# Performance work log

Hardware: AMD Instinct MI355X
Metric: run time of the kernel (lower is better)

## Reference

```python
import jax, jax.numpy as jnp
import numpy as np

B, T, D, H = 4, 1024, 1024, 16
DK = D // H
SCALE = float(np.sqrt(DK))


def setup_inputs() -> dict:
    key = jax.random.key(0)
    ks = jax.random.split(key, 12)
    std = 1.0 / np.sqrt(D)
    inp = {
        "x": jax.random.normal(ks[0], (B, T, D), dtype=jnp.float32),
        "s2_distances": jax.random.uniform(ks[1], (B, T, T), dtype=jnp.float32),
        # causal mask: 1 where attention allowed (j <= i)
        "mask": jnp.broadcast_to(jnp.tril(jnp.ones((T, T), dtype=jnp.int32)), (B, T, T)),
        "Wq": jax.random.uniform(ks[2], (D, D), jnp.float32, -std, std),
        "bq": jax.random.uniform(ks[3], (D,), jnp.float32, -std, std),
        "Wk": jax.random.uniform(ks[4], (D, D), jnp.float32, -std, std),
        "bk": jax.random.uniform(ks[5], (D,), jnp.float32, -std, std),
        "Wv": jax.random.uniform(ks[6], (D, D), jnp.float32, -std, std),
        "bv": jax.random.uniform(ks[7], (D,), jnp.float32, -std, std),
        "Wo": jax.random.uniform(ks[8], (D, D), jnp.float32, -std, std),
        "bo": jax.random.uniform(ks[9], (D,), jnp.float32, -std, std),
        "spatial_weight": jnp.float32(0.5),
    }
    return inp


def reference(x, s2_distances, mask, Wq, bq, Wk, bk, Wv, bv, Wo, bo, spatial_weight):
    b, t, _ = x.shape
    # projections: torch nn.Linear is x @ W.T + b
    def proj(W, bias):
        y = jnp.einsum("btd,ed->bte", x, W) + bias
        return y.reshape(b, t, H, DK).transpose(0, 2, 1, 3)  # [B,H,T,dk]

    Q, K, V = proj(Wq, bq), proj(Wk, bk), proj(Wv, bv)
    # scores: QK^T/sqrt(dk) - |alpha| * dist  (dist broadcast over heads)
    scores = jnp.einsum("bhqd,bhkd->bhqk", Q, K) / SCALE
    scores = scores - jnp.abs(spatial_weight) * s2_distances[:, None, :, :]
    scores = jnp.where(mask[:, None, :, :] == 0, -jnp.inf, scores)
    probs = jax.nn.softmax(scores, axis=-1)
    out = jnp.einsum("bhqk,bhkd->bhqd", probs, V)
    out = out.transpose(0, 2, 1, 3).reshape(b, t, D)
    return jnp.einsum("btd,ed->bte", out, Wo) + bo
```

## Files before the change

kernel.cpp:

```cpp
#include <hip/hip_runtime.h>
#include <stdint.h>

#define Tt 1024
#define Dd 1024
#define Hh 16
#define NT 32

typedef unsigned short u16;
typedef __attribute__((ext_vector_type(8))) short short8;
typedef __attribute__((ext_vector_type(4))) float f32x4;
typedef __attribute__((ext_vector_type(4))) unsigned short u16x4;

typedef const __attribute__((address_space(1))) uint32_t* gptr_t;
typedef __attribute__((address_space(3))) uint32_t* lptr_t;

#define QSCALE 0.18033688011112042f
#define LOG2E 1.4426950408889634f

static __device__ __forceinline__ u16 f2bf(float f) {
  union { float f; unsigned u; } x;
  x.f = f;
  unsigned u = x.u;
  return (u16)((u + 0x7fffu + ((u >> 16) & 1u)) >> 16);
}

static __device__ __forceinline__ u16 f2bf_fast(float f) {
  union { float f; unsigned u; } x;
  x.f = f;
  return (u16)((x.u + 0x8000u) >> 16);
}

static __device__ __forceinline__ float bf2f(u16 u) {
  union { unsigned u; float f; } x;
  x.u = ((unsigned)u) << 16;
  return x.f;
}

static __device__ __forceinline__ float fexp2(float x) {
#if __has_builtin(__builtin_amdgcn_exp2f)
  return __builtin_amdgcn_exp2f(x);
#else
  return exp2f(x);
#endif
}

__global__ __launch_bounds__(256) void cvt_kernel(
    const float* __restrict__ x, const float* __restrict__ wq,
    const float* __restrict__ wk, const float* __restrict__ wv,
    const float* __restrict__ wo, u16* __restrict__ xb, u16* __restrict__ wb) {
  size_t i = ((size_t)blockIdx.x * 256 + threadIdx.x) * 4;
  const size_t XN = (size_t)4 * 1024 * 1024;
  const float* src;
  u16* dst;
  size_t off;
  if (i < XN) {
    src = x; dst = xb; off = i;
  } else {
    size_t j = i - XN;
    int wi = (int)(j >> 20);
    src = (wi == 0) ? wq : (wi == 1) ? wk : (wi == 2) ? wv : wo;
    dst = wb + ((size_t)wi << 20);
    off = j & ((1u << 20) - 1);
  }
  float4 v = *(const float4*)(src + off);
  u16x4 o;
  o.x = f2bf(v.x); o.y = f2bf(v.y); o.z = f2bf(v.z); o.w = f2bf(v.w);
  *(u16x4*)(dst + off) = o;
}

__global__ __launch_bounds__(512, 2) void qkv_fused_kernel(
    const u16* __restrict__ xb, const u16* __restrict__ wb,
    const float* __restrict__ bq, const float* __restrict__ bk,
    const float* __restrict__ bv, u16* __restrict__ Q, u16* __restrict__ Kk,
    u16* __restrict__ Vt, const float* __restrict__ dist,
    const float* __restrict__ alphap, u16* __restrict__ biasb) {
  __shared__ u16 lds[65536];
  const int bid = blockIdx.x;
  const int xcd = bid & 7, cslot = bid >> 3;
  if (cslot >= 24) {
    const int cid = xcd * 8 + (cslot - 24);
    const float scl = -fabsf(alphap[0]) * LOG2E;
    const size_t idx = (size_t)cid * 512 + threadIdx.x;
#pragma unroll 4
    for (int i = 0; i < 32; i++) {
      const size_t off = idx * 4 + (size_t)i * 131072;
      float4 v = *(const float4*)(dist + off);
      u16x4 o;
      o.x = f2bf(v.x * scl); o.y = f2bf(v.y * scl);
      o.z = f2bf(v.z * scl); o.w = f2bf(v.w * scl);
      *(u16x4*)(biasb + off) = o;
    }
    return;
  }
  const int gid = xcd * 24 + cslot;
  const int mt = gid / 12, ny = gid - mt * 12;
  const int z = ny >> 2;
  const int m0 = mt * 256, nc = (ny & 3) * 256;
  const u16* W = wb + ((size_t)z << 20);

  const int t = threadIdx.x, w = t >> 6, l = t & 63;
  const int quad = l >> 4, l15 = l & 15;
  const int wr = w >> 2, wn = w & 3;
  char* ldc = (char*)lds;

  const int srow = t >> 2;
  const int scw = ((t & 3) ^ ((srow >> 1) & 3)) * 8;
  const u16* gA = xb + (size_t)(m0 + srow) * Dd + scw;
  const u16* gB = W + (size_t)(nc + srow) * Dd + scw;
  const int lb = w * 1024;

  auto stageA = [&](int kt, int u) {
    __builtin_amdgcn_global_load_lds(
        (gptr_t)(gA + (size_t)u * 128 * Dd + kt * 32),
        (lptr_t)(ldc + (kt & 3) * 32768 + u * 8192 + lb), 16, 0, 0);
  };
  auto stageB = [&](int kt, int u) {
    __builtin_amdgcn_global_load_lds(
        (gptr_t)(gB + (size_t)u * 128 * Dd + kt * 32),
        (lptr_t)(ldc + (kt & 3) * 32768 + 16384 + u * 8192 + lb), 16, 0, 0);
  };

  f32x4 acc[8][4];
#pragma unroll
  for (int i = 0; i < 8; i++)
#pragma unroll
    for (int j = 0; j < 4; j++) acc[i][j] = (f32x4){0.f, 0.f, 0.f, 0.f};

#pragma unroll
  for (int p = 0; p < 3; p++) {
    stageA(p, 0); stageA(p, 1); stageB(p, 0); stageB(p, 1);
  }
  asm volatile("s_waitcnt vmcnt(8)" ::: "memory");
  __builtin_amdgcn_s_barrier();

  const int rsw = (quad ^ ((l15 >> 1) & 3)) * 16;
  const int aoff = wr * 8192 + l15 * 64 + rsw;
  const int boff = 16384 + wn * 4096 + l15 * 64 + rsw;

#pragma unroll 1
  for (int kt = 0; kt < NT; kt++) {
    const char* sl = ldc + (kt & 3) * 32768;
    short8 af[4], bfv[4];
#pragma unroll
    for (int i = 0; i < 4; i++) af[i] = *(const short8*)(sl + aoff + i * 1024);
#pragma unroll
    for (int i = 0; i < 4; i++) bfv[i] = *(const short8*)(sl + boff + i * 1024);
    if (kt + 3 < NT) { stageA(kt + 3, 0); stageA(kt + 3, 1); }
    __builtin_amdgcn_s_barrier();
    asm volatile("s_waitcnt lgkmcnt(0)" ::: "memory");
    __builtin_amdgcn_sched_barrier(0);
    __builtin_amdgcn_s_setprio(1);
#pragma unroll
    for (int mi = 0; mi < 4; mi++)
#pragma unroll
      for (int ni = 0; ni < 4; ni++)
        acc[mi][ni] = __builtin_amdgcn_mfma_f32_16x16x32_bf16(
            af[mi], bfv[ni], acc[mi][ni], 0, 0, 0);
    __builtin_amdgcn_s_setprio(0);
    __builtin_amdgcn_s_barrier();
#pragma unroll
    for (int i = 0; i < 4; i++)
      af[i] = *(const short8*)(sl + aoff + 4096 + i * 1024);
    if (kt + 3 < NT) { stageB(kt + 3, 0); stageB(kt + 3, 1); }
    if (kt < NT - 3) {
      asm volatile("s_waitcnt vmcnt(8)" ::: "memory");
    } else if (kt == NT - 3) {
      asm volatile("s_waitcnt vmcnt(4)" ::: "memory");
    } else if (kt == NT - 2) {
      asm volatile("s_waitcnt vmcnt(0)" ::: "memory");
    }
    __builtin_amdgcn_s_barrier();
    asm volatile("s_waitcnt lgkmcnt(0)" ::: "memory");
    __builtin_amdgcn_sched_barrier(0);
    __builtin_amdgcn_s_setprio(1);
#pragma unroll
    for (int mi = 0; mi < 4; mi++)
#pragma unroll
      for (int ni = 0; ni < 4; ni++)
        acc[mi + 4][ni] = __builtin_amdgcn_mfma_f32_16x16x32_bf16(
            af[mi], bfv[ni], acc[mi + 4][ni], 0, 0, 0);
    __builtin_amdgcn_s_setprio(0);
    __builtin_amdgcn_s_barrier();
  }

  const float* bias = (z == 0) ? bq : (z == 1) ? bk : bv;
  const float scl = (z == 0) ? QSCALE : 1.0f;
  if (z < 2) {
#pragma unroll
    for (int mi = 0; mi < 8; mi++)
#pragma unroll
      for (int ni = 0; ni < 4; ni++) {
        const int n = wn * 64 + ni * 16 + l15;
        const float bn = bias[nc + n];
#pragma unroll
        for (int r = 0; r < 4; r++) {
          const int m = wr * 128 + mi * 16 + quad * 4 + r;
          lds[m * 256 + n] = f2bf((acc[mi][ni][r] + bn) * scl);
        }
      }
  } else {
#pragma unroll
    for (int mi = 0; mi < 8; mi++)
#pragma unroll
      for (int ni = 0; ni < 4; ni++) {
        const int n = wn * 64 + ni * 16 + l15;
        const float bn = bias[nc + n];
        u16x4 o;
        o.x = f2bf(acc[mi][ni][0] + bn);
        o.y = f2bf(acc[mi][ni][1] + bn);
        o.z = f2bf(acc[mi][ni][2] + bn);
        o.w = f2bf(acc[mi][ni][3] + bn);
        *(u16x4*)&lds[n * 256 + wr * 128 + mi * 16 + quad * 4] = o;
      }
  }
  __syncthreads();
  const int row = t >> 5;
  const int chunk = (t & 31) * 8;
  if (z < 2) {
    u16* out = (z == 0) ? Q : Kk;
#pragma unroll
    for (int it = 0; it < 16; it++) {
      const int rr = it * 16 + row;
      *(short8*)(out + (size_t)(m0 + rr) * Dd + nc + chunk) =
          *(const short8*)&lds[rr * 256 + chunk];
    }
  } else {
    const int b2 = m0 >> 10, t0 = m0 & (Tt - 1);
#pragma unroll
    for (int it = 0; it < 16; it++) {
      const int rr = it * 16 + row;
      *(short8*)(Vt + ((size_t)b2 * Dd + nc + rr) * Tt + t0 + chunk) =
          *(const short8*)&lds[rr * 256 + chunk];
    }
  }
}

__global__ __launch_bounds__(512) void gemm_out_kernel(
    const u16* __restrict__ Ao, const u16* __restrict__ Wo,
    const float* __restrict__ bo, float* __restrict__ out) {
  __shared__ u16 lds[2 * 12288];
  const int m0 = blockIdx.x * 128, n0 = blockIdx.y * 64;
  const int t = threadIdx.x, w = t >> 6, l = t & 63, quad = l >> 4, l15 = l & 15;
  const int srow = t >> 3;
  const int scol = ((l & 7) ^ ((l >> 3) & 7)) * 8;
  const u16* ga = Ao + (size_t)(m0 + srow) * Dd + scol;
  const u16* gb = Wo + (size_t)(n0 + srow) * Dd + scol;
  char* ldc = (char*)lds;
  const int xr = l15 & 7;
  f32x4 acc[4];
#pragma unroll
  for (int j = 0; j < 4; j++) acc[j] = (f32x4){0.f, 0.f, 0.f, 0.f};

  auto stage = [&](int k0, int buf) {
    char* base = ldc + buf * 24576 + w * 1024;
#pragma unroll
    for (int i = 0; i < 2; i++)
      __builtin_amdgcn_global_load_lds((gptr_t)(ga + k0 + (size_t)i * 64 * Dd),
                                       (lptr_t)(base + i * 8192), 16, 0, 0);
    __builtin_amdgcn_global_load_lds((gptr_t)(gb + k0),
                                     (lptr_t)(base + 16384), 16, 0, 0);
  };

  stage(0, 0);
#pragma unroll 1
  for (int it = 0; it < Dd / 64; it++) {
    const int buf = it & 1;
    __builtin_amdgcn_s_waitcnt(0);
    __syncthreads();
    if (it + 1 < Dd / 64) stage((it + 1) * 64, buf ^ 1);
    const u16* lA = lds + buf * 12288;
    const u16* lB = lA + 8192;
#pragma unroll
    for (int kk = 0; kk < 2; kk++) {
      const int cs = ((kk * 4 + quad) ^ xr) * 8;
      const short8 af = *(const short8*)(lA + (w * 16 + l15) * 64 + cs);
#pragma unroll
      for (int ni = 0; ni < 4; ni++) {
        const short8 bfr = *(const short8*)(lB + (ni * 16 + l15) * 64 + cs);
        acc[ni] = __builtin_amdgcn_mfma_f32_16x16x32_bf16(af, bfr, acc[ni], 0, 0, 0);
      }
    }
  }
#pragma unroll
  for (int ni = 0; ni < 4; ni++) {
    const int n = n0 + ni * 16 + l15;
    const float bn = bo[n];
#pragma unroll
    for (int r = 0; r < 4; r++) {
      const int m = m0 + w * 16 + quad * 4 + r;
      out[(size_t)m * Dd + n] = acc[ni][r] + bn;
    }
  }
}

__global__ __launch_bounds__(256) void attn_kernel(
    const u16* __restrict__ Q, const u16* __restrict__ Kk,
    const u16* __restrict__ Vt, const u16* __restrict__ biasb,
    u16* __restrict__ Oo) {
  __shared__ u16 lK[2][64 * 64];
  __shared__ u16 lV[2][64 * 64];
  __shared__ u16 lPp[4][16 * 64];
  const int t = threadIdx.x, w = t >> 6, l = t & 63, quad = l >> 4, l15 = l & 15;
  const int g = blockIdx.x >> 8;
  const int j = (blockIdx.x >> 6) & 3;
  const int bh = blockIdx.x & 63;
  const int qb = (g == 0) ? 15 - j : (g == 1) ? 8 + j : (g == 2) ? 7 - j : j;
  const int h = bh & (Hh - 1), b = bh >> 4;
  const int q0 = qb * 64;

  const int srow = w * 8 + (l >> 3);
  const int schunk = ((l & 7) ^ ((l >> 3) & 7)) * 8;
  const u16* gK = Kk + ((size_t)b * Tt + srow) * Dd + h * 64 + schunk;
  const u16* gV = Vt + ((size_t)b * Dd + h * 64 + srow) * Tt + schunk;
  char* lKc0 = (char*)&lK[0][0];
  char* lVc0 = (char*)&lV[0][0];
  const int wbase = w * 1024;

  auto stage = [&](int k0, int buf) {
#pragma unroll
    for (int i = 0; i < 2; i++) {
      __builtin_amdgcn_global_load_lds(
          (gptr_t)(gK + (size_t)(k0 + i * 32) * Dd),
          (lptr_t)(lKc0 + buf * 8192 + wbase + i * 4096), 16, 0, 0);
      __builtin_amdgcn_global_load_lds(
          (gptr_t)(gV + (size_t)(i * 32) * Tt + k0),
          (lptr_t)(lVc0 + buf * 8192 + wbase + i * 4096), 16, 0, 0);
    }
  };

  const int qrow = q0 + w * 16 + l15;
  const u16* Qp = Q + ((size_t)b * Tt + qrow) * Dd + h * 64 + quad * 8;
  const short8 qf0 = *(const short8*)Qp;
  const short8 qf1 = *(const short8*)(Qp + 32);
  const u16* bp = biasb + ((size_t)b * Tt + qrow) * Tt + quad * 4;

  const int xr = l15 & 7;
  u16* lpr = &lPp[w][l15 * 64];
  const int niter = qb + 1;

  f32x4 oacc[4];
#pragma unroll
  for (int dt = 0; dt < 4; dt++) oacc[dt] = (f32x4){0.f, 0.f, 0.f, 0.f};
  f32x4 lsum4 = (f32x4){0.f, 0.f, 0.f, 0.f};
  u16x4 bbA[4], bbB[4];

  stage(0, 0);
#pragma unroll
  for (int nt = 0; nt < 4; nt++) bbA[nt] = *(const u16x4*)(bp + nt * 16);

#pragma unroll 1
  for (int kt = 0; kt < niter; kt++) {
    const int buf = kt & 1;
    __builtin_amdgcn_s_waitcnt(0);
    __syncthreads();
    if (kt + 1 < niter) {
      stage((kt + 1) * 64, buf ^ 1);
#pragma unroll
      for (int nt = 0; nt < 4; nt++)
        bbB[nt] = *(const u16x4*)(bp + (kt + 1) * 64 + nt * 16);
    }
    f32x4 sacc[4];
#pragma unroll
    for (int nt = 0; nt < 4; nt++) {
#pragma unroll
      for (int r = 0; r < 4; r++) sacc[nt][r] = bf2f(bbA[nt][r]);
    }
#pragma unroll
    for (int ks = 0; ks < 2; ks++) {
      const short8 qf = ks ? qf1 : qf0;
      const int cs = ((ks * 4 + quad) ^ xr) * 8;
#pragma unroll
      for (int nt = 0; nt < 4; nt++) {
        const short8 kf = *(const short8*)&lK[buf][(nt * 16 + l15) * 64 + cs];
        sacc[nt] = __builtin_amdgcn_mfma_f32_16x16x32_bf16(kf, qf, sacc[nt], 0, 0, 0);
      }
    }
    if (kt == qb) {
      const int kbase = kt * 64 + quad * 4;
#pragma unroll
      for (int nt = 0; nt < 4; nt++) {
        u16x4 pk;
#pragma unroll
        for (int r = 0; r < 4; r++) {
          const float p = (kbase + nt * 16 + r <= qrow) ? fexp2(sacc[nt][r]) : 0.f;
          lsum4[nt] += p;
          pk[r] = f2bf_fast(p);
        }
        *(u16x4*)&lpr[((nt * 4 + quad) ^ (xr << 1)) * 4] = pk;
      }
    } else {
#pragma unroll
      for (int nt = 0; nt < 4; nt++) {
        u16x4 pk;
#pragma unroll
        for (int r = 0; r < 4; r++) {
          const float p = fexp2(sacc[nt][r]);
          lsum4[nt] += p;
          pk[r] = f2bf_fast(p);
        }
        *(u16x4*)&lpr[((nt * 4 + quad) ^ (xr << 1)) * 4] = pk;
      }
    }
#pragma unroll
    for (int ks = 0; ks < 2; ks++) {
      const int cs = ((ks * 4 + quad) ^ xr) * 8;
      const short8 pa = *(const short8*)&lpr[cs];
#pragma unroll
      for (int dt = 0; dt < 4; dt++) {
        const short8 vf = *(const short8*)&lV[buf][(dt * 16 + l15) * 64 + cs];
        oacc[dt] = __builtin_amdgcn_mfma_f32_16x16x32_bf16(pa, vf, oacc[dt], 0, 0, 0);
      }
    }
#pragma unroll
    for (int nt = 0; nt < 4; nt++) bbA[nt] = bbB[nt];
  }

  float lsum = (lsum4[0] + lsum4[1]) + (lsum4[2] + lsum4[3]);
  lsum += __shfl_xor(lsum, 16);
  lsum += __shfl_xor(lsum, 32);
  const float inv = 1.0f / lsum;
  float invq[4];
#pragma unroll
  for (int r = 0; r < 4; r++) invq[r] = __shfl(inv, quad * 4 + r);
#pragma unroll
  for (int dt = 0; dt < 4; dt++) {
#pragma unroll
    for (int r = 0; r < 4; r++) {
      Oo[((size_t)b * Tt + q0 + w * 16 + quad * 4 + r) * Dd + h * 64 + dt * 16 + l15] =
          f2bf(oacc[dt][r] * invq[r]);
    }
  }
}

extern "C" void kernel_launch(void* const* d_in, const int* in_sizes, int n_in,
                              void* d_out, int out_size, void* d_ws, size_t ws_size,
                              hipStream_t stream) {
  const float* x = (const float*)d_in[0];
  const float* dist = (const float*)d_in[1];
  const float* Wq = (const float*)d_in[3];
  const float* bq = (const float*)d_in[4];
  const float* Wk = (const float*)d_in[5];
  const float* bk = (const float*)d_in[6];
  const float* Wv = (const float*)d_in[7];
  const float* bv = (const float*)d_in[8];
  const float* Wo = (const float*)d_in[9];
  const float* bo = (const float*)d_in[10];
  const float* alphap = (const float*)d_in[11];

  char* ws = (char*)d_ws;
  u16* xb = (u16*)(ws);
  u16* wb = (u16*)(ws + ((size_t)8 << 20));
  u16* Qb = (u16*)(ws + ((size_t)16 << 20));
  u16* Kb = (u16*)(ws + ((size_t)24 << 20));
  u16* Vtb = (u16*)(ws + ((size_t)32 << 20));
  u16* biasb = (u16*)(ws + ((size_t)40 << 20));
  u16* Ob = xb;
  float* outp = (float*)d_out;

  cvt_kernel<<<8192, 256, 0, stream>>>(x, Wq, Wk, Wv, Wo, xb, wb);
  qkv_fused_kernel<<<256, 512, 0, stream>>>(xb, wb, bq, bk, bv, Qb, Kb, Vtb,
                                            dist, alphap, biasb);
  attn_kernel<<<1024, 256, 0, stream>>>(Qb, Kb, Vtb, biasb, Ob);
  dim3 g2(32, 16);
  gemm_out_kernel<<<g2, 512, 0, stream>>>(Ob, wb + ((size_t)3 << 20), bo, outp);
}
```

Measured before the change: 194.9 us.

## Move distance-bias conversion into cvt kernel and restructure QKV GEMM pipeline

The fp32-to-bf16 conversion of the scaled distance bias moves out of the QKV GEMM kernel's extra blocks and into the elementwise cvt kernel, which gets a larger grid. The QKV GEMM switches from a 4-stage K=32 ring with split A/B staging to a double-buffered K=64 tile with an XOR-swizzled 128-byte row layout. Its LDS epilogue stores are also swizzled to reduce bank conflicts. The prefetch depth drops from three tiles to one, so global latency may be less well hidden, while barrier overhead per K step is lower.

```diff
diff --git a/kernel.cpp b/kernel.cpp
--- a/kernel.cpp
+++ b/kernel.cpp
@@ -4,7 +4,6 @@
 #define Tt 1024
 #define Dd 1024
 #define Hh 16
-#define NT 32
 
 typedef unsigned short u16;
 typedef __attribute__((ext_vector_type(8))) short short8;
@@ -47,24 +46,32 @@
 __global__ __launch_bounds__(256) void cvt_kernel(
     const float* __restrict__ x, const float* __restrict__ wq,
     const float* __restrict__ wk, const float* __restrict__ wv,
-    const float* __restrict__ wo, u16* __restrict__ xb, u16* __restrict__ wb) {
+    const float* __restrict__ wo, const float* __restrict__ dist,
+    const float* __restrict__ alphap, u16* __restrict__ xb,
+    u16* __restrict__ wb, u16* __restrict__ biasb) {
   size_t i = ((size_t)blockIdx.x * 256 + threadIdx.x) * 4;
   const size_t XN = (size_t)4 * 1024 * 1024;
+  const size_t WN = (size_t)8 * 1024 * 1024;
+  float mul = 1.0f;
   const float* src;
   u16* dst;
   size_t off;
   if (i < XN) {
     src = x; dst = xb; off = i;
-  } else {
+  } else if (i < WN) {
     size_t j = i - XN;
     int wi = (int)(j >> 20);
     src = (wi == 0) ? wq : (wi == 1) ? wk : (wi == 2) ? wv : wo;
     dst = wb + ((size_t)wi << 20);
     off = j & ((1u << 20) - 1);
+  } else {
+    src = dist; dst = biasb; off = i - WN;
+    mul = -fabsf(alphap[0]) * LOG2E;
   }
   float4 v = *(const float4*)(src + off);
   u16x4 o;
-  o.x = f2bf(v.x); o.y = f2bf(v.y); o.z = f2bf(v.z); o.w = f2bf(v.w);
+  o.x = f2bf(v.x * mul); o.y = f2bf(v.y * mul);
+  o.z = f2bf(v.z * mul); o.w = f2bf(v.w * mul);
   *(u16x4*)(dst + off) = o;
 }
 
@@ -72,28 +79,10 @@
     const u16* __restrict__ xb, const u16* __restrict__ wb,
     const float* __restrict__ bq, const float* __restrict__ bk,
     const float* __restrict__ bv, u16* __restrict__ Q, u16* __restrict__ Kk,
-    u16* __restrict__ Vt, const float* __restrict__ dist,
-    const float* __restrict__ alphap, u16* __restrict__ biasb) {
+    u16* __restrict__ Vt) {
   __shared__ u16 lds[65536];
   const int bid = blockIdx.x;
-  const int xcd = bid & 7, cslot = bid >> 3;
-  if (cslot >= 24) {
-    const int cid = xcd * 8 + (cslot - 24);
-    const float scl = -fabsf(alphap[0]) * LOG2E;
-    const size_t idx = (size_t)cid * 512 + threadIdx.x;
-#pragma unroll 4
-    for (int i = 0; i < 32; i++) {
-      const size_t off = idx * 4 + (size_t)i * 131072;
-      float4 v = *(const float4*)(dist + off);
-      u16x4 o;
-      o.x = f2bf(v.x * scl); o.y = f2bf(v.y * scl);
-      o.z = f2bf(v.z * scl); o.w = f2bf(v.w * scl);
-      *(u16x4*)(biasb + off) = o;
-    }
-    return;
-  }
-  const int gid = xcd * 24 + cslot;
-  const int mt = gid / 12, ny = gid - mt * 12;
+  const int mt = bid & 15, ny = bid >> 4;
   const int z = ny >> 2;
   const int m0 = mt * 256, nc = (ny & 3) * 256;
   const u16* W = wb + ((size_t)z << 20);
@@ -103,22 +92,23 @@
   const int wr = w >> 2, wn = w & 3;
   char* ldc = (char*)lds;
 
-  const int srow = t >> 2;
-  const int scw = ((t & 3) ^ ((srow >> 1) & 3)) * 8;
-  const u16* gA = xb + (size_t)(m0 + srow) * Dd + scw;
-  const u16* gB = W + (size_t)(nc + srow) * Dd + scw;
+  const int srow = t >> 3;
+  const int schunk = ((t & 7) ^ (srow & 7)) * 8;
+  const u16* gA = xb + (size_t)(m0 + srow) * Dd + schunk;
+  const u16* gB = W + (size_t)(nc + srow) * Dd + schunk;
   const int lb = w * 1024;
 
-  auto stageA = [&](int kt, int u) {
-    __builtin_amdgcn_global_load_lds(
-        (gptr_t)(gA + (size_t)u * 128 * Dd + kt * 32),
-        (lptr_t)(ldc + (kt & 3) * 32768 + u * 8192 + lb), 16, 0, 0);
+  auto stage = [&](int kt, int buf) {
+#pragma unroll
+    for (int u = 0; u < 4; u++) {
+      __builtin_amdgcn_global_load_lds(
+          (gptr_t)(gA + (size_t)u * 64 * Dd + kt * 64),
+          (lptr_t)(ldc + buf * 65536 + u * 8192 + lb), 16, 0, 0);
+      __builtin_amdgcn_global_load_lds(
+          (gptr_t)(gB + (size_t)u * 64 * Dd + kt * 64),
+          (lptr_t)(ldc + buf * 65536 + 32768 + u * 8192 + lb), 16, 0, 0);
+    }
   };
-  auto stageB = [&](int kt, int u) {
-    __builtin_amdgcn_global_load_lds(
-        (gptr_t)(gB + (size_t)u * 128 * Dd + kt * 32),
-        (lptr_t)(ldc + (kt & 3) * 32768 + 16384 + u * 8192 + lb), 16, 0, 0);
-  };
 
   f32x4 acc[8][4];
 #pragma unroll
@@ -126,61 +116,41 @@
 #pragma unroll
     for (int j = 0; j < 4; j++) acc[i][j] = (f32x4){0.f, 0.f, 0.f, 0.f};
 
-#pragma unroll
-  for (int p = 0; p < 3; p++) {
-    stageA(p, 0); stageA(p, 1); stageB(p, 0); stageB(p, 1);
-  }
-  asm volatile("s_waitcnt vmcnt(8)" ::: "memory");
+  stage(0, 0);
+  asm volatile("s_waitcnt vmcnt(0)" ::: "memory");
   __builtin_amdgcn_s_barrier();
 
-  const int rsw = (quad ^ ((l15 >> 1) & 3)) * 16;
-  const int aoff = wr * 8192 + l15 * 64 + rsw;
-  const int boff = 16384 + wn * 4096 + l15 * 64 + rsw;
+  const int xr = l15 & 7;
 
 #pragma unroll 1
-  for (int kt = 0; kt < NT; kt++) {
-    const char* sl = ldc + (kt & 3) * 32768;
-    short8 af[4], bfv[4];
-#pragma unroll
-    for (int i = 0; i < 4; i++) af[i] = *(const short8*)(sl + aoff + i * 1024);
-#pragma unroll
-    for (int i = 0; i < 4; i++) bfv[i] = *(const short8*)(sl + boff + i * 1024);
-    if (kt + 3 < NT) { stageA(kt + 3, 0); stageA(kt + 3, 1); }
-    __builtin_amdgcn_s_barrier();
-    asm volatile("s_waitcnt lgkmcnt(0)" ::: "memory");
-    __builtin_amdgcn_sched_barrier(0);
-    __builtin_amdgcn_s_setprio(1);
-#pragma unroll
-    for (int mi = 0; mi < 4; mi++)
+  for (int kt = 0; kt < 16; kt++) {
+    const int buf = kt & 1;
+    const char* sl = ldc + buf * 65536;
+    if (kt + 1 < 16) stage(kt + 1, buf ^ 1);
+#pragma unroll
+    for (int ks = 0; ks < 2; ks++) {
+      short8 af[8], bfv[4];
+      const int cs = ((ks * 4 + quad) ^ xr) * 16;
+#pragma unroll
+      for (int mi = 0; mi < 8; mi++)
+        af[mi] = *(const short8*)(sl + (wr * 128 + mi * 16 + l15) * 128 + cs);
 #pragma unroll
       for (int ni = 0; ni < 4; ni++)
-        acc[mi][ni] = __builtin_amdgcn_mfma_f32_16x16x32_bf16(
-            af[mi], bfv[ni], acc[mi][ni], 0, 0, 0);
-    __builtin_amdgcn_s_setprio(0);
-    __builtin_amdgcn_s_barrier();
-#pragma unroll
-    for (int i = 0; i < 4; i++)
-      af[i] = *(const short8*)(sl + aoff + 4096 + i * 1024);
-    if (kt + 3 < NT) { stageB(kt + 3, 0); stageB(kt + 3, 1); }
-    if (kt < NT - 3) {
-      asm volatile("s_waitcnt vmcnt(8)" ::: "memory");
-    } else if (kt == NT - 3) {
-      asm volatile("s_waitcnt vmcnt(4)" ::: "memory");
-    } else if (kt == NT - 2) {
-      asm volatile("s_waitcnt vmcnt(0)" ::: "memory");
-    }
-    __builtin_amdgcn_s_barrier();
-    asm volatile("s_waitcnt lgkmcnt(0)" ::: "memory");
-    __builtin_amdgcn_sched_barrier(0);
-    __builtin_amdgcn_s_setprio(1);
-#pragma unroll
-    for (int mi = 0; mi < 4; mi++)
-#pragma unroll
-      for (int ni = 0; ni < 4; ni++)
-        acc[mi + 4][ni] = __builtin_amdgcn_mfma_f32_16x16x32_bf16(
-            af[mi], bfv[ni], acc[mi + 4][ni], 0, 0, 0);
-    __builtin_amdgcn_s_setprio(0);
-    __builtin_amdgcn_s_barrier();
+        bfv[ni] = *(const short8*)(sl + 32768 + (wn * 64 + ni * 16 + l15) * 128 + cs);
+      __builtin_amdgcn_s_barrier();
+      asm volatile("s_waitcnt lgkmcnt(0)" ::: "memory");
+      __builtin_amdgcn_sched_barrier(0);
+      __builtin_amdgcn_s_setprio(1);
+#pragma unroll
+      for (int mi = 0; mi < 8; mi++)
+#pragma unroll
+        for (int ni = 0; ni < 4; ni++)
+          acc[mi][ni] = __builtin_amdgcn_mfma_f32_16x16x32_bf16(
+              af[mi], bfv[ni], acc[mi][ni], 0, 0, 0);
+      __builtin_amdgcn_s_setprio(0);
+      if (ks == 1) asm volatile("s_waitcnt vmcnt(0)" ::: "memory");
+      __builtin_amdgcn_s_barrier();
+    }
   }
 
   const float* bias = (z == 0) ? bq : (z == 1) ? bk : bv;
@@ -192,10 +162,11 @@
       for (int ni = 0; ni < 4; ni++) {
         const int n = wn * 64 + ni * 16 + l15;
         const float bn = bias[nc + n];
+        const int nsw = n ^ (quad << 4);
 #pragma unroll
         for (int r = 0; r < 4; r++) {
           const int m = wr * 128 + mi * 16 + quad * 4 + r;
-          lds[m * 256 + n] = f2bf((acc[mi][ni][r] + bn) * scl);
+          lds[m * 256 + nsw] = f2bf((acc[mi][ni][r] + bn) * scl);
         }
       }
   } else {
@@ -210,27 +181,30 @@
         o.y = f2bf(acc[mi][ni][1] + bn);
         o.z = f2bf(acc[mi][ni][2] + bn);
         o.w = f2bf(acc[mi][ni][3] + bn);
-        *(u16x4*)&lds[n * 256 + wr * 128 + mi * 16 + quad * 4] = o;
+        const int mp = (wr * 128 + mi * 16 + quad * 4) ^ ((n & 7) * 8);
+        *(u16x4*)&lds[n * 256 + mp] = o;
       }
   }
   __syncthreads();
   const int row = t >> 5;
-  const int chunk = (t & 31) * 8;
+  const int c8 = (t & 31) * 8;
   if (z < 2) {
     u16* out = (z == 0) ? Q : Kk;
 #pragma unroll
     for (int it = 0; it < 16; it++) {
       const int rr = it * 16 + row;
-      *(short8*)(out + (size_t)(m0 + rr) * Dd + nc + chunk) =
-          *(const short8*)&lds[rr * 256 + chunk];
+      const int pos = c8 ^ ((((rr >> 2) & 3)) << 4);
+      *(short8*)(out + (size_t)(m0 + rr) * Dd + nc + c8) =
+          *(const short8*)&lds[rr * 256 + pos];
     }
   } else {
     const int b2 = m0 >> 10, t0 = m0 & (Tt - 1);
 #pragma unroll
     for (int it = 0; it < 16; it++) {
       const int rr = it * 16 + row;
-      *(short8*)(Vt + ((size_t)b2 * Dd + nc + rr) * Tt + t0 + chunk) =
-          *(const short8*)&lds[rr * 256 + chunk];
+      const int pos = c8 ^ ((rr & 7) * 8);
+      *(short8*)(Vt + ((size_t)b2 * Dd + nc + rr) * Tt + t0 + c8) =
+          *(const short8*)&lds[rr * 256 + pos];
     }
   }
 }
@@ -457,9 +431,9 @@
   u16* Ob = xb;
   float* outp = (float*)d_out;
 
-  cvt_kernel<<<8192, 256, 0, stream>>>(x, Wq, Wk, Wv, Wo, xb, wb);
-  qkv_fused_kernel<<<256, 512, 0, stream>>>(xb, wb, bq, bk, bv, Qb, Kb, Vtb,
-                                            dist, alphap, biasb);
+  cvt_kernel<<<12288, 256, 0, stream>>>(x, Wq, Wk, Wv, Wo, dist, alphap,
+                                        xb, wb, biasb);
+  qkv_fused_kernel<<<192, 512, 0, stream>>>(xb, wb, bq, bk, bv, Qb, Kb, Vtb);
   attn_kernel<<<1024, 256, 0, stream>>>(Qb, Kb, Vtb, biasb, Ob);
   dim3 g2(32, 16);
   gemm_out_kernel<<<g2, 512, 0, stream>>>(Ob, wb + ((size_t)3 << 20), bo, outp);
```

After: 197.8 us. No clear change (+1.5%).
